# Optimization experiments

Measured on AMD Instinct MI355X. Metric: run time of the kernel, lower is better.

The kernel has to match this reference:

```python
import jax, jax.numpy as jnp
import numpy as np

NUM_SCOPE = 64
NUM_SAMPLE = 16
DIM_ENCODE = 64


def _fixed_basis(dim):
    # FixedTimeEncoder / FixedFrequencyEncoder basis: w_i = 1 / 10^(9*i/(dim-1))
    return (1.0 / 10.0 ** jnp.linspace(0.0, 9.0, dim)).astype(jnp.float32)


def _cos_encode(t, dim):
    # t: [...] -> [..., dim]
    w = _fixed_basis(dim)
    return jnp.cos(t[..., None] * w)


def setup_inputs() -> dict:
    key = jax.random.key(0)
    ks = jax.random.split(key, 12)
    n, b, df = 4096, NUM_SCOPE, 172
    s_in = 1.0 / np.sqrt(df)
    return {
        "root_node_feature": jax.random.normal(ks[0], (n, df), jnp.float32),
        "root_ts": jax.random.uniform(ks[1], (n,), jnp.float32) * 1e4,
        "neighbor_node_feature": jax.random.normal(ks[2], (n, b, df), jnp.float32),
        "neighbor_edge_feature": jax.random.normal(ks[3], (n, b, df), jnp.float32),
        "neighbor_ts": jax.random.uniform(ks[4], (n, b), jnp.float32) * 1e4,
        "neighbor_nid": jax.random.randint(ks[5], (n, b), 0, 10000, jnp.int64) if jax.config.jax_enable_x64 else jax.random.randint(ks[5], (n, b), 0, 10000, jnp.int32),
        "W_node": jax.random.normal(ks[6], (df, 64), jnp.float32) * s_in,
        "b_node": jnp.zeros((64,), jnp.float32),
        "W_edge": jax.random.normal(ks[7], (df, 64), jnp.float32) * s_in,
        "b_edge": jnp.zeros((64,), jnp.float32),
        "W_link": jax.random.normal(ks[8], (320, 256), jnp.float32) / np.sqrt(320),
        "W_root": jax.random.normal(ks[9], (192, 256), jnp.float32) / np.sqrt(192),
    }


def reference(root_node_feature, root_ts, neighbor_node_feature,
              neighbor_edge_feature, neighbor_ts, neighbor_nid,
              W_node, b_node, W_edge, b_edge, W_link, W_root):
    n, b = neighbor_nid.shape
    # --- encode root node ---
    root_feat = jax.nn.relu(root_node_feature @ W_node + b_node)          # [n,64]
    root_time = _cos_encode(jnp.zeros((n,), jnp.float32), DIM_ENCODE)     # [n,64]
    root_freq = _cos_encode(jnp.ones((n,), jnp.float32), DIM_ENCODE)      # [n,64]
    root_encode = jnp.concatenate([root_feat, root_time, root_freq], 1)   # [n,192]
    # --- encode links ---
    node_enc = jax.nn.relu(neighbor_node_feature @ W_node + b_node)       # [n,b,64]
    edge_enc = jax.nn.relu(neighbor_edge_feature @ W_edge + b_edge)       # [n,b,64]
    neigh_time = root_ts[:, None] - neighbor_ts                           # [n,b]
    time_enc = _cos_encode(neigh_time, DIM_ENCODE)                        # [n,b,64]
    # pairwise equality mask + frequency count (keep_dummy_freq=True)
    neigh_mask = (neighbor_nid[:, :, None] == neighbor_nid[:, None, :])   # [n,b,b]
    neigh_freq = neigh_mask.sum(-1).astype(jnp.float32) / NUM_SCOPE       # [n,b]
    freq_enc = _cos_encode(neigh_freq, DIM_ENCODE)                        # [n,b,64]
    iden_enc = neigh_mask.astype(jnp.float32)                             # [n,b,b]
    link_encode = jnp.concatenate(
        [node_enc, edge_enc, time_enc, freq_enc, iden_enc], axis=-1)      # [n,b,320]
    # --- link mapper: project links & root, score, softmax over neighbors ---
    h_link = jax.nn.relu(jnp.einsum('nbd,dh->nbh', link_encode, W_link))  # [n,b,256]
    h_root = jax.nn.relu(root_encode @ W_root)                            # [n,256]
    scores = jnp.einsum('nbh,nh->nb', h_link, h_root) / jnp.sqrt(256.0)
    probs = jax.nn.softmax(scores, axis=-1)                               # [n,b]
    # --- weighted sampling WITHOUT replacement via Gumbel top-k ---
    g = jax.random.gumbel(jax.random.key(42), (n, b), jnp.float32)
    logp = jnp.log(probs + 1e-20)
    _, action = jax.lax.top_k(logp + g, NUM_SAMPLE)                       # [n,num_sample]
    return probs, action
```

## Files before the change

### kernel.cpp

```cpp
#include <hip/hip_runtime.h>
#include <cstdint>
#include <math.h>

#define B       64
#define DF      172
#define HDIM    256
#define KSAMP   16
#define THREADS 512

#define FMA4(A_, S_, W_) \
  A_.x = fmaf(S_, W_.x, A_.x); A_.y = fmaf(S_, W_.y, A_.y); \
  A_.z = fmaf(S_, W_.z, A_.z); A_.w = fmaf(S_, W_.w, A_.w);

__device__ __forceinline__ uint32_t rotl32(uint32_t x, int d) {
  return (x << d) | (x >> (32 - d));
}

__device__ __forceinline__ void threefry2x32(uint32_t k0, uint32_t k1,
                                             uint32_t& x0, uint32_t& x1) {
  const uint32_t ks0 = k0, ks1 = k1, ks2 = k0 ^ k1 ^ 0x1BD11BDAu;
  x0 += ks0; x1 += ks1;
#define TF_R4(ra,rb,rc,rd) \
  x0 += x1; x1 = rotl32(x1, ra); x1 ^= x0; \
  x0 += x1; x1 = rotl32(x1, rb); x1 ^= x0; \
  x0 += x1; x1 = rotl32(x1, rc); x1 ^= x0; \
  x0 += x1; x1 = rotl32(x1, rd); x1 ^= x0;
  TF_R4(13,15,26,6)  x0 += ks1; x1 += ks2 + 1u;
  TF_R4(17,29,16,24) x0 += ks2; x1 += ks0 + 2u;
  TF_R4(13,15,26,6)  x0 += ks0; x1 += ks1 + 3u;
  TF_R4(17,29,16,24) x0 += ks1; x1 += ks2 + 4u;
  TF_R4(13,15,26,6)  x0 += ks2; x1 += ks0 + 5u;
#undef TF_R4
}

#define ENC_FMA(W0_, W1_, W2_, W3_, X0_, X1_) { \
  FMA4(acc0, X0_.x, W0_) FMA4(acc0, X0_.y, W1_) FMA4(acc0, X0_.z, W2_) FMA4(acc0, X0_.w, W3_) \
  FMA4(acc1, X1_.x, W0_) FMA4(acc1, X1_.y, W1_) FMA4(acc1, X1_.z, W2_) FMA4(acc1, X1_.w, W3_) }

__device__ __forceinline__ void enc_gemm_g(const float* __restrict__ gA,
                                           const float* __restrict__ W,
                                           const float* __restrict__ bias,
                                           float* __restrict__ out,
                                           int b2, int cg) {
  const float4* W4 = (const float4*)W;
  const float4* A0 = (const float4*)(gA + (size_t)(2 * b2) * DF);
  const float4* A1 = (const float4*)(gA + (size_t)(2 * b2 + 1) * DF);
  float4 acc0 = ((const float4*)bias)[cg];
  float4 acc1 = acc0;
  float4 w0 = W4[0 * 16 + cg], w1 = W4[1 * 16 + cg];
  float4 w2 = W4[2 * 16 + cg], w3 = W4[3 * 16 + cg];
  float4 x0 = A0[0], x1 = A1[0];
  for (int k = 0; k < DF; k += 4) {
    const float4 wa = w0, wb = w1, wc = w2, wd = w3;
    const float4 xa = x0, xb = x1;
    if (k < DF - 4) {
      w0 = W4[(k + 4) * 16 + cg]; w1 = W4[(k + 5) * 16 + cg];
      w2 = W4[(k + 6) * 16 + cg]; w3 = W4[(k + 7) * 16 + cg];
      x0 = A0[(k >> 2) + 1];      x1 = A1[(k >> 2) + 1];
    }
    ENC_FMA(wa, wb, wc, wd, xa, xb)
  }
  float4 o0 = make_float4(fmaxf(acc0.x, 0.f), fmaxf(acc0.y, 0.f), fmaxf(acc0.z, 0.f), fmaxf(acc0.w, 0.f));
  float4 o1 = make_float4(fmaxf(acc1.x, 0.f), fmaxf(acc1.y, 0.f), fmaxf(acc1.z, 0.f), fmaxf(acc1.w, 0.f));
  ((float4*)out)[(2 * b2) * 16 + cg]     = o0;
  ((float4*)out)[(2 * b2 + 1) * 16 + cg] = o1;
}

__device__ __forceinline__ void accum16(float2 (&acc)[16],
                                        const float* __restrict__ enc, int r16,
                                        const float2* __restrict__ Wlp) {
  float2 w0 = Wlp[0], w1 = Wlp[128], w2 = Wlp[256], w3 = Wlp[384];
  for (int d0 = 0; d0 < 64; d0 += 4) {
    const float2 wa = w0, wb = w1, wc = w2, wd = w3;
    if (d0 < 60) {
      const float2* p = Wlp + (d0 + 4) * 128;
      w0 = p[0]; w1 = p[128]; w2 = p[256]; w3 = p[384];
    }
#pragma unroll
    for (int i = 0; i < 16; ++i) {
      const float4 e = *(const float4*)&enc[(r16 + i) * 64 + d0];
      acc[i].x = fmaf(e.x, wa.x, acc[i].x); acc[i].y = fmaf(e.x, wa.y, acc[i].y);
      acc[i].x = fmaf(e.y, wb.x, acc[i].x); acc[i].y = fmaf(e.y, wb.y, acc[i].y);
      acc[i].x = fmaf(e.z, wc.x, acc[i].x); acc[i].y = fmaf(e.z, wc.y, acc[i].y);
      acc[i].x = fmaf(e.w, wd.x, acc[i].x); acc[i].y = fmaf(e.w, wd.y, acc[i].y);
    }
  }
}

__global__ __launch_bounds__(THREADS, 4)
void AdaptSampler_kernel(const float* __restrict__ rootf,
                         const float* __restrict__ root_ts,
                         const float* __restrict__ nf,
                         const float* __restrict__ ef,
                         const float* __restrict__ nts,
                         const int*   __restrict__ nid,
                         const float* __restrict__ Wn,
                         const float* __restrict__ bn,
                         const float* __restrict__ We,
                         const float* __restrict__ be,
                         const float* __restrict__ Wl,
                         const float* __restrict__ Wr,
                         float* __restrict__ out_probs,
                         float* __restrict__ out_action)
{
  __shared__ float encA[B * 64];
  __shared__ float encB[B * 64];
  __shared__ float encC[B * 64];
  __shared__ float hroot_lds[HDIM];
  __shared__ float rootenc_lds[192];
  __shared__ float w_lds[B];
  __shared__ float ts_lds[B];
  __shared__ __align__(16) int nid_lds[B];
  __shared__ float freq_lds[B];
  __shared__ unsigned long long mask_lds[B];
  __shared__ float scpart[4][16][2];

  const int n = blockIdx.x;
  const int t = threadIdx.x;
  const int c2  = t & 127;
  const int r16 = (t >> 7) * 16;
  const int b2 = t >> 4;
  const int cg = t & 15;
  const float2* Wl2 = (const float2*)Wl;

  if (t >= 448) {
    const int j = t - 448;
    double e = 9.0 * (double)j / 63.0;
    const float wj = (float)(1.0 / pow(10.0, e));
    w_lds[j]   = wj;
    nid_lds[j] = nid[n * B + j];
    ts_lds[j]  = nts[n * B + j];
    float a = bn[j];
    const float* rr = rootf + (size_t)n * DF;
#pragma unroll 4
    for (int d = 0; d < DF; ++d) a = fmaf(rr[d], Wn[d * 64 + j], a);
    rootenc_lds[j]       = fmaxf(a, 0.0f);
    rootenc_lds[64 + j]  = 1.0f;
    rootenc_lds[128 + j] = cosf(wj);
    const int my = nid_lds[j];
    unsigned long long m = 0ull;
    for (int k = 0; k < B; ++k)
      m |= ((unsigned long long)(nid_lds[k] == my)) << k;
    mask_lds[j] = m;
    freq_lds[j] = (float)__popcll(m) * 0.015625f;
  }
  __syncthreads();

  enc_gemm_g(nf + (size_t)n * B * DF, Wn, bn, encA, b2, cg);
  __builtin_amdgcn_sched_barrier(0);
  enc_gemm_g(ef + (size_t)n * B * DF, We, be, encC, b2, cg);
  __builtin_amdgcn_sched_barrier(0);
  {
    const float rts = root_ts[n];
#pragma unroll
    for (int q = 0; q < 8; ++q) {
      const int idx = q * 512 + t;
      const int bb = idx >> 6, dd = idx & 63;
      encB[idx] = cosf((rts - ts_lds[bb]) * w_lds[dd]);
    }
  }
  {
    const int h = t >> 1, hf = t & 1;
    float a = 0.0f;
    for (int d = hf * 96; d < hf * 96 + 96; ++d)
      a = fmaf(rootenc_lds[d], Wr[d * HDIM + h], a);
    a += __shfl_xor(a, 1);
    if (hf == 0) hroot_lds[h] = fmaxf(a, 0.0f);
  }
  __syncthreads();

  float2 acc[16];
#pragma unroll
  for (int i = 0; i < 16; ++i) acc[i] = make_float2(0.f, 0.f);
  accum16(acc, encA, r16, Wl2 + c2);
  __builtin_amdgcn_sched_barrier(0);
  accum16(acc, encC, r16, Wl2 + 64 * 128 + c2);
  __builtin_amdgcn_sched_barrier(0);
  accum16(acc, encB, r16, Wl2 + 128 * 128 + c2);
  __syncthreads();

#pragma unroll
  for (int q = 0; q < 8; ++q) {
    const int idx = q * 512 + t;
    const int bb = idx >> 6, dd = idx & 63;
    encB[idx] = cosf(freq_lds[bb] * w_lds[dd]);
  }
  __syncthreads();

  accum16(acc, encB, r16, Wl2 + 192 * 128 + c2);
  {
    const float2* Wlp = Wl2 + 256 * 128 + c2;
#pragma unroll
    for (int i = 0; i < 16; ++i) {
      unsigned long long m = mask_lds[r16 + i];
      while (m) {
        const int d = __builtin_ctzll(m);
        m &= m - 1;
        const float2 wv = Wlp[d * 128];
        acc[i].x += wv.x;
        acc[i].y += wv.y;
      }
    }
  }
  {
    const float2 hr = ((const float2*)hroot_lds)[c2];
#pragma unroll
    for (int i = 0; i < 16; ++i) {
      float s = fmaxf(acc[i].x, 0.f) * hr.x;
      s = fmaf(fmaxf(acc[i].y, 0.f), hr.y, s);
#pragma unroll
      for (int mm = 32; mm >= 1; mm >>= 1) s += __shfl_xor(s, mm);
      if ((t & 63) == 0) scpart[t >> 7][i][(t >> 6) & 1] = s;
    }
  }
  __syncthreads();

  if (t < B) {
    float s = (scpart[t >> 4][t & 15][0] + scpart[t >> 4][t & 15][1]) * 0.0625f;
    float m = s;
#pragma unroll
    for (int mm = 32; mm >= 1; mm >>= 1) m = fmaxf(m, __shfl_xor(m, mm));
    float e = expf(s - m);
    float sum = e;
#pragma unroll
    for (int mm = 32; mm >= 1; mm >>= 1) sum += __shfl_xor(sum, mm);
    float p = e / sum;
    out_probs[(size_t)n * B + t] = p;

    uint32_t i = (uint32_t)(n * B + t);
    uint32_t x0 = 0u, x1 = i;
    threefry2x32(0u, 42u, x0, x1);
    uint32_t bits = x0 ^ x1;
    float f = __uint_as_float((bits >> 9) | 0x3f800000u) - 1.0f;
    const float TINY = 1.1754943508222875e-38f;
    float u = fmaxf(f * (1.0f - TINY) + TINY, TINY);
    float g = -logf(-logf(u));
    float keyv = logf(p + 1e-20f) + g;

    float v = keyv;
    for (int k = 0; k < KSAMP; ++k) {
      float bv = v; int bi = t;
#pragma unroll
      for (int mm = 32; mm >= 1; mm >>= 1) {
        float ov = __shfl_xor(bv, mm);
        int   oi = __shfl_xor(bi, mm);
        if (ov > bv || (ov == bv && oi < bi)) { bv = ov; bi = oi; }
      }
      if (t == 0) out_action[(size_t)n * KSAMP + k] = (float)bi;
      if (t == bi) v = -3.402823466e+38f;
    }
  }
}

extern "C" void kernel_launch(void* const* d_in, const int* in_sizes, int n_in,
                              void* d_out, int out_size, void* d_ws, size_t ws_size,
                              hipStream_t stream) {
  const float* rootf = (const float*)d_in[0];
  const float* rts   = (const float*)d_in[1];
  const float* nf    = (const float*)d_in[2];
  const float* ef    = (const float*)d_in[3];
  const float* nts   = (const float*)d_in[4];
  const int*   nid   = (const int*)d_in[5];
  const float* Wn    = (const float*)d_in[6];
  const float* bn    = (const float*)d_in[7];
  const float* We    = (const float*)d_in[8];
  const float* be    = (const float*)d_in[9];
  const float* Wl    = (const float*)d_in[10];
  const float* Wr    = (const float*)d_in[11];

  const int n = in_sizes[1];
  float* probs  = (float*)d_out;
  float* action = probs + (size_t)n * B;

  AdaptSampler_kernel<<<dim3(n), dim3(THREADS), 0, stream>>>(
      rootf, rts, nf, ef, nts, nid, Wn, bn, We, be, Wl, Wr, probs, action);
}
```

Measured before the change: 1.045 ms.

## Restructure kernel into per-wave row ownership with async global-to-LDS feature staging

Each of the 8 waves now owns 8 neighbor rows end to end. It stages that slice of node and edge features into LDS with global_load_lds, computes the encoder outputs and the full 256-wide link projection for its rows, and builds the identity masks with wave ballots. This removes most block-wide barriers and the separate encA/B/C buffers, and it overlaps the edge-feature load with the node encoder. In exchange, every wave redundantly computes the root encoding, LDS use grows to about 44KB, and launch bounds drop to 2 blocks per SM, which may reduce occupancy.

Measured after the change: 1.052 ms. No clear change (+0.7%).

```diff
diff --git a/kernel.cpp b/kernel.cpp
--- a/kernel.cpp
+++ b/kernel.cpp
@@ -7,6 +7,9 @@
 #define HDIM    256
 #define KSAMP   16
 #define THREADS 512
+
+typedef const __attribute__((address_space(1))) unsigned int* gp_t;
+typedef __attribute__((address_space(3))) unsigned int* lp_t;
 
 #define FMA4(A_, S_, W_) \
   A_.x = fmaf(S_, W_.x, A_.x); A_.y = fmaf(S_, W_.y, A_.y); \
@@ -33,61 +36,45 @@
 #undef TF_R4
 }
 
-#define ENC_FMA(W0_, W1_, W2_, W3_, X0_, X1_) { \
-  FMA4(acc0, X0_.x, W0_) FMA4(acc0, X0_.y, W1_) FMA4(acc0, X0_.z, W2_) FMA4(acc0, X0_.w, W3_) \
-  FMA4(acc1, X1_.x, W0_) FMA4(acc1, X1_.y, W1_) FMA4(acc1, X1_.z, W2_) FMA4(acc1, X1_.w, W3_) }
-
-__device__ __forceinline__ void enc_gemm_g(const float* __restrict__ gA,
-                                           const float* __restrict__ W,
-                                           const float* __restrict__ bias,
-                                           float* __restrict__ out,
-                                           int b2, int cg) {
-  const float4* W4 = (const float4*)W;
-  const float4* A0 = (const float4*)(gA + (size_t)(2 * b2) * DF);
-  const float4* A1 = (const float4*)(gA + (size_t)(2 * b2 + 1) * DF);
-  float4 acc0 = ((const float4*)bias)[cg];
-  float4 acc1 = acc0;
-  float4 w0 = W4[0 * 16 + cg], w1 = W4[1 * 16 + cg];
-  float4 w2 = W4[2 * 16 + cg], w3 = W4[3 * 16 + cg];
-  float4 x0 = A0[0], x1 = A1[0];
-  for (int k = 0; k < DF; k += 4) {
+__device__ __forceinline__ void enc_wp(const float* __restrict__ Arow,
+                                       const float4* __restrict__ Wp,
+                                       const float4* __restrict__ bp,
+                                       float* __restrict__ outRow, int cg8) {
+  float4 lo = bp[0], hi = bp[1];
+  float4 w0 = Wp[0], w1 = Wp[1];
+  float  a0 = Arow[0];
+  for (int k = 0; k < DF; ++k) {
+    const float4 wa = w0, wb = w1; const float av = a0;
+    if (k < DF - 1) {
+      w0 = Wp[(k + 1) * 16]; w1 = Wp[(k + 1) * 16 + 1]; a0 = Arow[k + 1];
+    }
+    FMA4(lo, av, wa) FMA4(hi, av, wb)
+  }
+  float4 o0 = make_float4(fmaxf(lo.x, 0.f), fmaxf(lo.y, 0.f), fmaxf(lo.z, 0.f), fmaxf(lo.w, 0.f));
+  float4 o1 = make_float4(fmaxf(hi.x, 0.f), fmaxf(hi.y, 0.f), fmaxf(hi.z, 0.f), fmaxf(hi.w, 0.f));
+  ((float4*)outRow)[cg8 * 2]     = o0;
+  ((float4*)outRow)[cg8 * 2 + 1] = o1;
+}
+
+__device__ __forceinline__ void accum_wp(float4 (&acc)[8],
+                                         const float* __restrict__ eb,
+                                         const float4* __restrict__ Wlp) {
+  float4 w0 = Wlp[0], w1 = Wlp[64], w2 = Wlp[128], w3 = Wlp[192];
+  for (int d0 = 0; d0 < 64; d0 += 4) {
     const float4 wa = w0, wb = w1, wc = w2, wd = w3;
-    const float4 xa = x0, xb = x1;
-    if (k < DF - 4) {
-      w0 = W4[(k + 4) * 16 + cg]; w1 = W4[(k + 5) * 16 + cg];
-      w2 = W4[(k + 6) * 16 + cg]; w3 = W4[(k + 7) * 16 + cg];
-      x0 = A0[(k >> 2) + 1];      x1 = A1[(k >> 2) + 1];
-    }
-    ENC_FMA(wa, wb, wc, wd, xa, xb)
-  }
-  float4 o0 = make_float4(fmaxf(acc0.x, 0.f), fmaxf(acc0.y, 0.f), fmaxf(acc0.z, 0.f), fmaxf(acc0.w, 0.f));
-  float4 o1 = make_float4(fmaxf(acc1.x, 0.f), fmaxf(acc1.y, 0.f), fmaxf(acc1.z, 0.f), fmaxf(acc1.w, 0.f));
-  ((float4*)out)[(2 * b2) * 16 + cg]     = o0;
-  ((float4*)out)[(2 * b2 + 1) * 16 + cg] = o1;
-}
-
-__device__ __forceinline__ void accum16(float2 (&acc)[16],
-                                        const float* __restrict__ enc, int r16,
-                                        const float2* __restrict__ Wlp) {
-  float2 w0 = Wlp[0], w1 = Wlp[128], w2 = Wlp[256], w3 = Wlp[384];
-  for (int d0 = 0; d0 < 64; d0 += 4) {
-    const float2 wa = w0, wb = w1, wc = w2, wd = w3;
     if (d0 < 60) {
-      const float2* p = Wlp + (d0 + 4) * 128;
-      w0 = p[0]; w1 = p[128]; w2 = p[256]; w3 = p[384];
-    }
-#pragma unroll
-    for (int i = 0; i < 16; ++i) {
-      const float4 e = *(const float4*)&enc[(r16 + i) * 64 + d0];
-      acc[i].x = fmaf(e.x, wa.x, acc[i].x); acc[i].y = fmaf(e.x, wa.y, acc[i].y);
-      acc[i].x = fmaf(e.y, wb.x, acc[i].x); acc[i].y = fmaf(e.y, wb.y, acc[i].y);
-      acc[i].x = fmaf(e.z, wc.x, acc[i].x); acc[i].y = fmaf(e.z, wc.y, acc[i].y);
-      acc[i].x = fmaf(e.w, wd.x, acc[i].x); acc[i].y = fmaf(e.w, wd.y, acc[i].y);
-    }
-  }
-}
-
-__global__ __launch_bounds__(THREADS, 4)
+      const float4* p = Wlp + (d0 + 4) * 64;
+      w0 = p[0]; w1 = p[64]; w2 = p[128]; w3 = p[192];
+    }
+#pragma unroll
+    for (int i = 0; i < 8; ++i) {
+      const float4 e = *(const float4*)&eb[i * 64 + d0];
+      FMA4(acc[i], e.x, wa) FMA4(acc[i], e.y, wb) FMA4(acc[i], e.z, wc) FMA4(acc[i], e.w, wd)
+    }
+  }
+}
+
+__global__ __launch_bounds__(THREADS, 2)
 void AdaptSampler_kernel(const float* __restrict__ rootf,
                          const float* __restrict__ root_ts,
                          const float* __restrict__ nf,
@@ -103,120 +90,126 @@
                          float* __restrict__ out_probs,
                          float* __restrict__ out_action)
 {
-  __shared__ float encA[B * 64];
-  __shared__ float encB[B * 64];
-  __shared__ float encC[B * 64];
+  __shared__ float S_lds[B * DF];
+  __shared__ float encW[B * 64];
+  __shared__ float rootenc[8][192];
   __shared__ float hroot_lds[HDIM];
-  __shared__ float rootenc_lds[192];
-  __shared__ float w_lds[B];
-  __shared__ float ts_lds[B];
-  __shared__ __align__(16) int nid_lds[B];
-  __shared__ float freq_lds[B];
-  __shared__ unsigned long long mask_lds[B];
-  __shared__ float scpart[4][16][2];
+  __shared__ float sc_lds[B];
 
   const int n = blockIdx.x;
   const int t = threadIdx.x;
-  const int c2  = t & 127;
-  const int r16 = (t >> 7) * 16;
-  const int b2 = t >> 4;
-  const int cg = t & 15;
-  const float2* Wl2 = (const float2*)Wl;
-
-  if (t >= 448) {
-    const int j = t - 448;
-    double e = 9.0 * (double)j / 63.0;
-    const float wj = (float)(1.0 / pow(10.0, e));
-    w_lds[j]   = wj;
-    nid_lds[j] = nid[n * B + j];
-    ts_lds[j]  = nts[n * B + j];
-    float a = bn[j];
+  const int w = t >> 6;
+  const int l = t & 63;
+  const int rloc = l >> 3;
+  const int cg8  = l & 7;
+
+  float* Sw = S_lds + w * (8 * DF);
+  float* ew = encW  + w * (8 * 64);
+
+  const float* gnf = nf + (size_t)n * B * DF + (size_t)w * 8 * DF;
+#pragma unroll
+  for (int j = 0; j < 5; ++j)
+    __builtin_amdgcn_global_load_lds((gp_t)(gnf + j * 256 + l * 4), (lp_t)(Sw + j * 256), 16, 0, 0);
+  if (l < 24)
+    __builtin_amdgcn_global_load_lds((gp_t)(gnf + 1280 + l * 4), (lp_t)(Sw + 1280), 16, 0, 0);
+
+  const int   nid_l = nid[n * B + l];
+  const float ts_l  = nts[n * B + l];
+  const float rts   = root_ts[n];
+  const float w_l   = (float)(1.0 / pow(10.0, 9.0 * (double)l / 63.0));
+
+  {
+    float rf = bn[l];
     const float* rr = rootf + (size_t)n * DF;
 #pragma unroll 4
-    for (int d = 0; d < DF; ++d) a = fmaf(rr[d], Wn[d * 64 + j], a);
-    rootenc_lds[j]       = fmaxf(a, 0.0f);
-    rootenc_lds[64 + j]  = 1.0f;
-    rootenc_lds[128 + j] = cosf(wj);
-    const int my = nid_lds[j];
-    unsigned long long m = 0ull;
-    for (int k = 0; k < B; ++k)
-      m |= ((unsigned long long)(nid_lds[k] == my)) << k;
-    mask_lds[j] = m;
-    freq_lds[j] = (float)__popcll(m) * 0.015625f;
-  }
-  __syncthreads();
-
-  enc_gemm_g(nf + (size_t)n * B * DF, Wn, bn, encA, b2, cg);
+    for (int d = 0; d < DF; ++d) rf = fmaf(rr[d], Wn[d * 64 + l], rf);
+    rootenc[w][l]       = fmaxf(rf, 0.0f);
+    rootenc[w][64 + l]  = 1.0f;
+    rootenc[w][128 + l] = cosf(w_l);
+  }
+
+  asm volatile("s_waitcnt vmcnt(0)" ::: "memory");
   __builtin_amdgcn_sched_barrier(0);
-  enc_gemm_g(ef + (size_t)n * B * DF, We, be, encC, b2, cg);
-  __builtin_amdgcn_sched_barrier(0);
-  {
-    const float rts = root_ts[n];
-#pragma unroll
-    for (int q = 0; q < 8; ++q) {
-      const int idx = q * 512 + t;
-      const int bb = idx >> 6, dd = idx & 63;
-      encB[idx] = cosf((rts - ts_lds[bb]) * w_lds[dd]);
-    }
-  }
+  enc_wp(Sw + rloc * DF, (const float4*)Wn + cg8 * 2, (const float4*)bn + cg8 * 2,
+         ew + rloc * 64, cg8);
+
+  const float* gef = ef + (size_t)n * B * DF + (size_t)w * 8 * DF;
+#pragma unroll
+  for (int j = 0; j < 5; ++j)
+    __builtin_amdgcn_global_load_lds((gp_t)(gef + j * 256 + l * 4), (lp_t)(Sw + j * 256), 16, 0, 0);
+  if (l < 24)
+    __builtin_amdgcn_global_load_lds((gp_t)(gef + 1280 + l * 4), (lp_t)(Sw + 1280), 16, 0, 0);
+
   {
     const int h = t >> 1, hf = t & 1;
     float a = 0.0f;
     for (int d = hf * 96; d < hf * 96 + 96; ++d)
-      a = fmaf(rootenc_lds[d], Wr[d * HDIM + h], a);
+      a = fmaf(rootenc[w][d], Wr[d * HDIM + h], a);
     a += __shfl_xor(a, 1);
     if (hf == 0) hroot_lds[h] = fmaxf(a, 0.0f);
   }
-  __syncthreads();
-
-  float2 acc[16];
-#pragma unroll
-  for (int i = 0; i < 16; ++i) acc[i] = make_float2(0.f, 0.f);
-  accum16(acc, encA, r16, Wl2 + c2);
+
+  float4 acc[8];
+#pragma unroll
+  for (int i = 0; i < 8; ++i) acc[i] = make_float4(0.f, 0.f, 0.f, 0.f);
+  accum_wp(acc, ew, (const float4*)Wl + l);
+
+  asm volatile("s_waitcnt vmcnt(0)" ::: "memory");
   __builtin_amdgcn_sched_barrier(0);
-  accum16(acc, encC, r16, Wl2 + 64 * 128 + c2);
-  __builtin_amdgcn_sched_barrier(0);
-  accum16(acc, encB, r16, Wl2 + 128 * 128 + c2);
-  __syncthreads();
+  enc_wp(Sw + rloc * DF, (const float4*)We + cg8 * 2, (const float4*)be + cg8 * 2,
+         ew + rloc * 64, cg8);
+  accum_wp(acc, ew, (const float4*)Wl + 64 * 64 + l);
 
 #pragma unroll
   for (int q = 0; q < 8; ++q) {
-    const int idx = q * 512 + t;
-    const int bb = idx >> 6, dd = idx & 63;
-    encB[idx] = cosf(freq_lds[bb] * w_lds[dd]);
-  }
-  __syncthreads();
-
-  accum16(acc, encB, r16, Wl2 + 192 * 128 + c2);
-  {
-    const float2* Wlp = Wl2 + 256 * 128 + c2;
-#pragma unroll
-    for (int i = 0; i < 16; ++i) {
-      unsigned long long m = mask_lds[r16 + i];
+    const float tsq = __shfl(ts_l, w * 8 + q);
+    ew[q * 64 + l] = cosf((rts - tsq) * w_l);
+  }
+  accum_wp(acc, ew, (const float4*)Wl + 128 * 64 + l);
+
+  unsigned long long mq[8];
+#pragma unroll
+  for (int q = 0; q < 8; ++q) {
+    const int nr = __shfl(nid_l, w * 8 + q);
+    mq[q] = __ballot(nid_l == nr);
+    const float fq = (float)__popcll(mq[q]) * 0.015625f;
+    ew[q * 64 + l] = cosf(fq * w_l);
+  }
+  accum_wp(acc, ew, (const float4*)Wl + 192 * 64 + l);
+
+  {
+    const float4* Wli = (const float4*)Wl + 256 * 64 + l;
+#pragma unroll
+    for (int q = 0; q < 8; ++q) {
+      unsigned long long m = mq[q];
       while (m) {
         const int d = __builtin_ctzll(m);
         m &= m - 1;
-        const float2 wv = Wlp[d * 128];
-        acc[i].x += wv.x;
-        acc[i].y += wv.y;
+        const float4 wv = Wli[d * 64];
+        acc[q].x += wv.x; acc[q].y += wv.y; acc[q].z += wv.z; acc[q].w += wv.w;
       }
     }
   }
-  {
-    const float2 hr = ((const float2*)hroot_lds)[c2];
-#pragma unroll
-    for (int i = 0; i < 16; ++i) {
-      float s = fmaxf(acc[i].x, 0.f) * hr.x;
-      s = fmaf(fmaxf(acc[i].y, 0.f), hr.y, s);
+
+  __syncthreads();
+
+  {
+    const float4 hrv = ((const float4*)hroot_lds)[l];
+#pragma unroll
+    for (int q = 0; q < 8; ++q) {
+      float s = fmaxf(acc[q].x, 0.f) * hrv.x;
+      s = fmaf(fmaxf(acc[q].y, 0.f), hrv.y, s);
+      s = fmaf(fmaxf(acc[q].z, 0.f), hrv.z, s);
+      s = fmaf(fmaxf(acc[q].w, 0.f), hrv.w, s);
 #pragma unroll
       for (int mm = 32; mm >= 1; mm >>= 1) s += __shfl_xor(s, mm);
-      if ((t & 63) == 0) scpart[t >> 7][i][(t >> 6) & 1] = s;
+      if (l == 0) sc_lds[w * 8 + q] = s;
     }
   }
   __syncthreads();
 
   if (t < B) {
-    float s = (scpart[t >> 4][t & 15][0] + scpart[t >> 4][t & 15][1]) * 0.0625f;
+    float s = sc_lds[t] * 0.0625f;
     float m = s;
 #pragma unroll
     for (int mm = 32; mm >= 1; mm >>= 1) m = fmaxf(m, __shfl_xor(m, mm));
```
